# Performance work log

Measured on AMD Instinct MI355X. Metric: run time of the kernel, lower is better.

Reference implementation:

```python
import jax, jax.numpy as jnp
import numpy as np

EPS = 1e-8  # matches torch F.cosine_similarity default eps


def _flatten_spatial(x):
    # [B, C, d, h, w] -> [B, N, C]
    B, C = x.shape[:2]
    return x.reshape(B, C, -1).transpose(0, 2, 1)


def _stage_loss(canon_src, canon_tgt, src_desc, tgt_desc):
    stage_size = src_desc.shape[2:]
    B, C = canon_src.shape[:2]
    # trilinear resize with half-pixel centers == torch align_corners=False
    rs = jax.image.resize(canon_src, (B, C) + stage_size, method='trilinear')
    rt = jax.image.resize(canon_tgt, (B, C) + stage_size, method='trilinear')
    a = _flatten_spatial(rs)  # [B, N, 3]
    b = _flatten_spatial(rt)  # [B, N, 3]
    # squared euclidean distances (argmin is invariant to sqrt)
    a2 = jnp.sum(a * a, axis=-1)  # [B, N]
    b2 = jnp.sum(b * b, axis=-1)  # [B, N]
    ab = jnp.einsum('bnc,bmc->bnm', a, b)  # [B, N, N]
    d2 = a2[:, :, None] + b2[:, None, :] - 2.0 * ab
    nearest = jnp.argmin(d2, axis=-1)  # [B, N] int
    sd = _flatten_spatial(src_desc)  # [B, N, Cd]
    td = _flatten_spatial(tgt_desc)  # [B, N, Cd]
    gathered = jnp.take_along_axis(td, nearest[:, :, None], axis=1)  # [B, N, Cd]
    num = jnp.sum(sd * gathered, axis=-1)
    denom = jnp.maximum(jnp.linalg.norm(sd, axis=-1), EPS) * \
            jnp.maximum(jnp.linalg.norm(gathered, axis=-1), EPS)
    cos = num / denom
    return 1.0 - jnp.mean(cos)


def setup_inputs() -> dict:
    key = jax.random.key(0)
    ks = jax.random.split(key, 6)
    return {
        'canonical_source': jax.random.normal(ks[0], (4, 3, 64, 64, 64), jnp.float32),
        'canonical_target': jax.random.normal(ks[1], (4, 3, 64, 64, 64), jnp.float32),
        'src_desc0': jax.random.normal(ks[2], (4, 32, 16, 16, 16), jnp.float32),
        'tgt_desc0': jax.random.normal(ks[3], (4, 32, 16, 16, 16), jnp.float32),
        'src_desc1': jax.random.normal(ks[4], (4, 32, 8, 8, 8), jnp.float32),
        'tgt_desc1': jax.random.normal(ks[5], (4, 32, 8, 8, 8), jnp.float32),
    }


def reference(canonical_source, canonical_target, src_desc0, tgt_desc0, src_desc1, tgt_desc1):
    l0 = _stage_loss(canonical_source, canonical_target, src_desc0, tgt_desc0)
    l1 = _stage_loss(canonical_source, canonical_target, src_desc1, tgt_desc1)
    return jnp.stack([l0, l1]).mean()
```

## Files before the change

kernel.cpp:

```cpp
#include <hip/hip_runtime.h>
#include <cfloat>

typedef unsigned long long u64;

#define CDESC 32
#define N0 4096
#define N1 512

__device__ __forceinline__ unsigned fbits_mono(float d) {
    unsigned b = __float_as_uint(d);
    return (d >= 0.f) ? (b | 0x80000000u) : ~b;
}

__device__ __forceinline__ void wave_reduce_atomic(float v, float* acc) {
#pragma unroll
    for (int off = 32; off > 0; off >>= 1) v += __shfl_down(v, off, 64);
    if ((threadIdx.x & 63) == 0) atomicAdd(acc, v);
}

__global__ __launch_bounds__(256) void pass1_fused(
        const float* __restrict__ csrc, const float* __restrict__ ctgt,
        const float* __restrict__ sd0, const float* __restrict__ td0,
        const float* __restrict__ sd1, const float* __restrict__ td1,
        float* __restrict__ x16a, float* __restrict__ x16b,
        float* __restrict__ x8a,  float* __restrict__ x8b,
        float* __restrict__ sd0T, float* __restrict__ td0T,
        float* __restrict__ sd1T, float* __restrict__ td1T,
        float* __restrict__ acc) {
    __shared__ __align__(16) float lds[6612];
    float* sRowP = lds;
    float* xf16P = lds + 4672;
    float* xf8P  = lds + 5964;
    const int tid = threadIdx.x;
    const int bx  = blockIdx.x, by = blockIdx.y;
    if (by == 0 && bx == 0 && tid < 4) acc[tid] = 0.f;

    if (bx < 768) {
        int bc = bx >> 6, z = bx & 63;
        const float* in = by ? ctgt : csrc;
        float* o16 = by ? x16b : x16a;
        float* o8  = by ? x8b  : x8a;
        if (tid < 512) {
            int r = tid >> 3, c = tid & 7;
            sRowP[r * 73 + (c < 4 ? c : 64 + c)] = 0.f;
        }
        if (tid < 76) {
            int r = tid / 19, c = tid % 19;
            xf16P[(r < 2 ? r : r + 64) * 19 + c] = 0.f;
        }
        if (tid < 72) {
            int r = tid / 9, c = tid % 9;
            xf8P[(r < 4 ? r : r + 64) * 9 + c] = 0.f;
        }
        const float4* src = (const float4*)(in + (size_t)(bc * 64 + z) * 4096);
#pragma unroll
        for (int k = 0; k < 4; ++k) {
            float4 v = src[tid + k * 256];
            int g = tid + k * 256;
            int y = g >> 4, j = (g & 15) * 4;
            float* p = &sRowP[y * 73 + 4 + j];
            p[0] = v.x; p[1] = v.y; p[2] = v.z; p[3] = v.w;
        }
        __syncthreads();
#pragma unroll
        for (int k = 0; k < 6; ++k) {
            int o = tid + k * 256;
            if (o < 1024) {
                int y = o >> 4, xo = o & 15;
                const float* r = &sRowP[y * 73 + 4 * xo + 2];
                float sum = 0.f;
#pragma unroll
                for (int t = 0; t < 8; ++t) {
                    float w = 1.f - fabsf((float)t - 3.5f) * 0.25f;
                    sum = fmaf(w, r[t], sum);
                }
                float wsum = (xo == 0 || xo == 15) ? 3.5f : 4.0f;
                xf16P[(y + 2) * 19 + xo] = sum / wsum;
            } else {
                int o2 = o - 1024;
                int y = o2 >> 3, xo = o2 & 7;
                const float* r = &sRowP[y * 73 + 8 * xo];
                float sum = 0.f;
#pragma unroll
                for (int t = 0; t < 16; ++t) {
                    float w = 1.f - fabsf((float)t - 7.5f) * 0.125f;
                    sum = fmaf(w, r[t], sum);
                }
                float wsum = (xo == 0 || xo == 7) ? 7.f : 8.f;
                xf8P[(y + 4) * 9 + xo] = sum / wsum;
            }
        }
        __syncthreads();
        {
            int y2 = tid >> 4, x = tid & 15;
            float sum = 0.f;
#pragma unroll
            for (int t = 0; t < 8; ++t) {
                float w = 1.f - fabsf((float)t - 3.5f) * 0.25f;
                sum = fmaf(w, xf16P[(4 * y2 + t) * 19 + x], sum);
            }
            float wsum = (y2 == 0 || y2 == 15) ? 3.5f : 4.0f;
            o16[bc * 16384 + z * 256 + y2 * 16 + x] = sum / wsum;
        }
        if (tid < 64) {
            int y2 = tid >> 3, x = tid & 7;
            float sum = 0.f;
#pragma unroll
            for (int t = 0; t < 16; ++t) {
                float w = 1.f - fabsf((float)t - 7.5f) * 0.125f;
                sum = fmaf(w, xf8P[(8 * y2 + t) * 9 + x], sum);
            }
            float wsum = (y2 == 0 || y2 == 7) ? 7.f : 8.f;
            o8[bc * 4096 + z * 64 + y2 * 8 + x] = sum / wsum;
        }
    } else {
        float* tile = lds;
        int tl = bx - 768;
        const float* din; float* dout; int N, b, n0;
        if (tl < 256) { din = by ? td0 : sd0; dout = by ? td0T : sd0T;
                        N = N0; b = tl >> 6; n0 = (tl & 63) * 64; }
        else { tl -= 256; din = by ? td1 : sd1; dout = by ? td1T : sd1T;
               N = N1; b = tl >> 3; n0 = (tl & 7) * 64; }
#pragma unroll
        for (int i = 0; i < 8; ++i) {
            int idx = tid + i * 256;
            int c = idx >> 6, j = idx & 63;
            tile[j * 33 + c] = din[((size_t)b * CDESC + c) * N + n0 + j];
        }
        __syncthreads();
#pragma unroll
        for (int i = 0; i < 8; ++i) {
            int idx = tid + i * 256;
            int p = idx >> 5, c = idx & 31;
            dout[((size_t)b * N + n0 + p) * CDESC + c] = tile[p * 33 + c];
        }
    }
}

__global__ __launch_bounds__(256) void pass2z(
        const float* __restrict__ x16a, const float* __restrict__ x16b,
        const float* __restrict__ x8a,  const float* __restrict__ x8b,
        float4* __restrict__ ps0, float4* __restrict__ pt0,
        float4* __restrict__ ps1, float4* __restrict__ pt1) {
    int gid = blockIdx.x * 256 + threadIdx.x;
    if (blockIdx.x < 128) {
        int side = gid >> 14, r = gid & 16383;
        int b = r >> 12, n = r & 4095;
        int x = n & 15, y = (n >> 4) & 15, z = n >> 8;
        const float* t = side ? x16b : x16a;
        const float* base = t + (size_t)b * 49152 + y * 16 + x;
        float a0 = 0.f, a1 = 0.f, a2 = 0.f, wzs = 0.f;
#pragma unroll
        for (int tt = 0; tt < 8; ++tt) {
            float w = 1.f - fabsf((float)tt - 3.5f) * 0.25f;
            int jz = 4 * z - 2 + tt;
            if ((unsigned)jz < 64u) {
                const float* p = base + jz * 256;
                a0 = fmaf(w, p[0],     a0);
                a1 = fmaf(w, p[16384], a1);
                a2 = fmaf(w, p[32768], a2);
                wzs += w;
            }
        }
        float inv = 1.f / wzs;
        a0 *= inv; a1 *= inv; a2 *= inv;
        float sq = a0 * a0 + a1 * a1 + a2 * a2;
        if (side) pt0[b * N0 + n] = make_float4(-2.f * a0, -2.f * a1, -2.f * a2, sq);
        else      ps0[b * N0 + n] = make_float4(a0, a1, a2, sq);
    } else {
        int g = gid - 32768;
        int side = g >> 11, r = g & 2047;
        int b = r >> 9, n = r & 511;
        int x = n & 7, y = (n >> 3) & 7, z = n >> 6;
        const float* t = side ? x8b : x8a;
        const float* base = t + (size_t)b * 12288 + y * 8 + x;
        float a0 = 0.f, a1 = 0.f, a2 = 0.f, wzs = 0.f;
#pragma unroll
        for (int tt = 0; tt < 16; ++tt) {
            float w = 1.f - fabsf((float)tt - 7.5f) * 0.125f;
            int jz = 8 * z - 4 + tt;
            if ((unsigned)jz < 64u) {
                const float* p = base + jz * 64;
                a0 = fmaf(w, p[0],    a0);
                a1 = fmaf(w, p[4096], a1);
                a2 = fmaf(w, p[8192], a2);
                wzs += w;
            }
        }
        float inv = 1.f / wzs;
        a0 *= inv; a1 *= inv; a2 *= inv;
        float sq = a0 * a0 + a1 * a1 + a2 * a2;
        if (side) pt1[b * N1 + n] = make_float4(-2.f * a0, -2.f * a1, -2.f * a2, sq);
        else      ps1[b * N1 + n] = make_float4(a0, a1, a2, sq);
    }
}

__device__ __forceinline__ float cos_pm(const float* __restrict__ sT,
                                        const float* __restrict__ tT,
                                        size_t si, size_t ti) {
    const float4* s = (const float4*)(sT + si * CDESC);
    const float4* t = (const float4*)(tT + ti * CDESC);
    float num = 0.f, s2 = 0.f, t2 = 0.f;
#pragma unroll
    for (int c = 0; c < 8; ++c) {
        float4 a = s[c], g = t[c];
        num = fmaf(a.x, g.x, fmaf(a.y, g.y, fmaf(a.z, g.z, fmaf(a.w, g.w, num))));
        s2  = fmaf(a.x, a.x, fmaf(a.y, a.y, fmaf(a.z, a.z, fmaf(a.w, a.w, s2))));
        t2  = fmaf(g.x, g.x, fmaf(g.y, g.y, fmaf(g.z, g.z, fmaf(g.w, g.w, t2))));
    }
    return num / (fmaxf(sqrtf(s2), 1e-8f) * fmaxf(sqrtf(t2), 1e-8f));
}

__device__ __forceinline__ float dist_pm(float4 P, float4 Q) {
    return fmaf(P.x, Q.x, fmaf(P.y, Q.y, fmaf(P.z, Q.z, Q.w)));
}

__global__ __launch_bounds__(256) void nn_cos_all(
        const float4* __restrict__ ps0, const float4* __restrict__ pt0,
        const float* __restrict__ sd0T, const float* __restrict__ td0T,
        const float4* __restrict__ ps1, const float4* __restrict__ pt1,
        const float* __restrict__ sd1T, const float* __restrict__ td1T,
        float* acc, float* __restrict__ out) {
    extern __shared__ __align__(16) char smraw[];
    float4* sm = (float4*)smraw;
    const int tid = threadIdx.x;
    const int bx  = blockIdx.x;

    if (bx < 256) {
        int b = bx >> 6, ptile = bx & 63;
        const float4* tp = pt0 + b * N0;
        for (int i = tid; i < N0; i += 256)
            sm[i] = tp[i];
        __syncthreads();
        int w = tid >> 6, lane = tid & 63;
        int n = ptile * 64 + lane;
        float4 P = ps0[b * N0 + n];
        const int m0 = w * 1024;
        float best = FLT_MAX; int bbase = 0;
        for (int k0 = 0; k0 < 1024; k0 += 16) {
            float d[16];
#pragma unroll
            for (int u = 0; u < 16; ++u)
                d[u] = dist_pm(P, sm[m0 + k0 + u]);
            float e0 = fminf(d[0],  d[1]),  e1 = fminf(d[2],  d[3]);
            float e2 = fminf(d[4],  d[5]),  e3 = fminf(d[6],  d[7]);
            float e4 = fminf(d[8],  d[9]),  e5 = fminf(d[10], d[11]);
            float e6 = fminf(d[12], d[13]), e7 = fminf(d[14], d[15]);
            float f0 = fminf(e0, e1), f1 = fminf(e2, e3);
            float f2 = fminf(e4, e5), f3 = fminf(e6, e7);
            float bm = fminf(fminf(f0, f1), fminf(f2, f3));
            if (bm < best) { best = bm; bbase = k0; }
        }
        int bi = 0;
#pragma unroll
        for (int u = 15; u >= 0; --u) {
            float dv = dist_pm(P, sm[m0 + bbase + u]);
            if (dv == best) bi = u;
        }
        u64 key = ((u64)fbits_mono(best) << 32) | (unsigned)(m0 + bbase + bi);
        __syncthreads();
        u64* keys = (u64*)smraw;
        keys[w * 64 + lane] = key;
        __syncthreads();
        if (tid < 64) {
            u64 k0 = keys[tid],       k1 = keys[tid + 64];
            u64 k2 = keys[tid + 128], k3 = keys[tid + 192];
            u64 ka = k0 < k1 ? k0 : k1;
            u64 kb = k2 < k3 ? k2 : k3;
            u64 kk = ka < kb ? ka : kb;
            int nearest = (int)(unsigned)(kk & 0xFFFFFFFFull);
            int n2 = ptile * 64 + tid;
            float cosv = cos_pm(sd0T, td0T, (size_t)b * N0 + n2,
                                (size_t)b * N0 + nearest);
            wave_reduce_atomic(cosv, acc + 0);
        }
    } else {
        int bb = bx - 256;
        int b = bb >> 1;
        const float4* tp = pt1 + b * N1;
        for (int i = tid; i < N1; i += 256)
            sm[i] = tp[i];
        __syncthreads();
        int n = (bb & 1) * 256 + tid;
        float4 P = ps1[b * N1 + n];
        float best = FLT_MAX; int bbase = 0;
        for (int k0 = 0; k0 < N1; k0 += 16) {
            float d[16];
#pragma unroll
            for (int u = 0; u < 16; ++u)
                d[u] = dist_pm(P, sm[k0 + u]);
            float e0 = fminf(d[0],  d[1]),  e1 = fminf(d[2],  d[3]);
            float e2 = fminf(d[4],  d[5]),  e3 = fminf(d[6],  d[7]);
            float e4 = fminf(d[8],  d[9]),  e5 = fminf(d[10], d[11]);
            float e6 = fminf(d[12], d[13]), e7 = fminf(d[14], d[15]);
            float f0 = fminf(e0, e1), f1 = fminf(e2, e3);
            float f2 = fminf(e4, e5), f3 = fminf(e6, e7);
            float bm = fminf(fminf(f0, f1), fminf(f2, f3));
            if (bm < best) { best = bm; bbase = k0; }
        }
        int bi = 0;
#pragma unroll
        for (int u = 15; u >= 0; --u) {
            float dv = dist_pm(P, sm[bbase + u]);
            if (dv == best) bi = u;
        }
        float cosv = cos_pm(sd1T, td1T, (size_t)b * N1 + n,
                            (size_t)b * N1 + bbase + bi);
        wave_reduce_atomic(cosv, acc + 1);
    }

    __syncthreads();
    if (tid == 0) {
        __threadfence();
        unsigned old = atomicAdd((unsigned*)(acc + 2), 1u);
        if (old == 263u) {
            float a0 = atomicAdd(acc + 0, 0.f);
            float a1 = atomicAdd(acc + 1, 0.f);
            out[0] = 1.f - 0.5f * (a0 * (1.f / 16384.f) + a1 * (1.f / 2048.f));
        }
    }
}

extern "C" void kernel_launch(void* const* d_in, const int* in_sizes, int n_in,
                              void* d_out, int out_size, void* d_ws, size_t ws_size,
                              hipStream_t stream) {
    const float* c_src = (const float*)d_in[0];
    const float* c_tgt = (const float*)d_in[1];
    const float* sd0   = (const float*)d_in[2];
    const float* td0   = (const float*)d_in[3];
    const float* sd1   = (const float*)d_in[4];
    const float* td1   = (const float*)d_in[5];
    float* out = (float*)d_out;

    char* ws = (char*)d_ws;
    float* acc  = (float*)ws;
    float* x16a = (float*)(ws + 256);
    float* x16b = x16a + 196608;
    float* x8a  = x16b + 196608;
    float* x8b  = x8a + 49152;
    float4* ps0 = (float4*)(x8b + 49152);
    float4* pt0 = ps0 + 16384;
    float4* ps1 = pt0 + 16384;
    float4* pt1 = ps1 + 2048;
    float* sd0T = (float*)(pt1 + 2048);
    float* td0T = sd0T + 524288;
    float* sd1T = td0T + 524288;
    float* td1T = sd1T + 65536;

    pass1_fused<<<dim3(1056, 2), 256, 0, stream>>>(c_src, c_tgt, sd0, td0, sd1, td1,
                                                   x16a, x16b, x8a, x8b,
                                                   sd0T, td0T, sd1T, td1T, acc);
    pass2z<<<144, 256, 0, stream>>>(x16a, x16b, x8a, x8b, ps0, pt0, ps1, pt1);
    nn_cos_all<<<264, 256, 65536, stream>>>(ps0, pt0, sd0T, td0T, ps1, pt1,
                                            sd1T, td1T, acc, out);
}
```

Baseline: 114.0 us.

## Split stage-0 NN search across blocks with 4-point register tiling and global atomicMin

Each stage-0 block now loads only a quarter of the target points (1024) into shared memory and has each thread evaluate four source points against one shared Q. This cuts LDS traffic per distance and shrinks dynamic shared memory. Partial argmins are merged through a global 64-bit atomicMin on packed keys, and a per-group ticket counter lets the last arriving block compute the cosine terms. Key and ticket initialization are folded into pass2z. The cost is global atomics and a last-block-done pattern that relies on memory visibility between blocks.

```diff
diff --git a/kernel.cpp b/kernel.cpp
--- a/kernel.cpp
+++ b/kernel.cpp
@@ -141,8 +141,11 @@
         const float* __restrict__ x16a, const float* __restrict__ x16b,
         const float* __restrict__ x8a,  const float* __restrict__ x8b,
         float4* __restrict__ ps0, float4* __restrict__ pt0,
-        float4* __restrict__ ps1, float4* __restrict__ pt1) {
+        float4* __restrict__ ps1, float4* __restrict__ pt1,
+        u64* __restrict__ gkeys, unsigned* __restrict__ gtick) {
     int gid = blockIdx.x * 256 + threadIdx.x;
+    if (gid < 16384) gkeys[gid] = ~0ull;
+    else if (gid < 16448) gtick[gid - 16384] = 0u;
     if (blockIdx.x < 128) {
         int side = gid >> 14, r = gid & 16383;
         int b = r >> 12, n = r & 4095;
@@ -220,56 +223,63 @@
         const float* __restrict__ sd0T, const float* __restrict__ td0T,
         const float4* __restrict__ ps1, const float4* __restrict__ pt1,
         const float* __restrict__ sd1T, const float* __restrict__ td1T,
+        u64* __restrict__ gkeys, unsigned* __restrict__ gtick,
         float* acc, float* __restrict__ out) {
     extern __shared__ __align__(16) char smraw[];
     float4* sm = (float4*)smraw;
+    __shared__ unsigned sflag;
     const int tid = threadIdx.x;
     const int bx  = blockIdx.x;
 
     if (bx < 256) {
-        int b = bx >> 6, ptile = bx & 63;
-        const float4* tp = pt0 + b * N0;
-        for (int i = tid; i < N0; i += 256)
+        int b = bx >> 6, g = (bx >> 2) & 15, q = bx & 3;
+        const float4* tp = pt0 + b * N0 + q * 1024;
+        for (int i = tid; i < 1024; i += 256)
             sm[i] = tp[i];
-        __syncthreads();
-        int w = tid >> 6, lane = tid & 63;
-        int n = ptile * 64 + lane;
-        float4 P = ps0[b * N0 + n];
-        const int m0 = w * 1024;
-        float best = FLT_MAX; int bbase = 0;
-        for (int k0 = 0; k0 < 1024; k0 += 16) {
-            float d[16];
-#pragma unroll
-            for (int u = 0; u < 16; ++u)
-                d[u] = dist_pm(P, sm[m0 + k0 + u]);
-            float e0 = fminf(d[0],  d[1]),  e1 = fminf(d[2],  d[3]);
-            float e2 = fminf(d[4],  d[5]),  e3 = fminf(d[6],  d[7]);
-            float e4 = fminf(d[8],  d[9]),  e5 = fminf(d[10], d[11]);
-            float e6 = fminf(d[12], d[13]), e7 = fminf(d[14], d[15]);
-            float f0 = fminf(e0, e1), f1 = fminf(e2, e3);
-            float f2 = fminf(e4, e5), f3 = fminf(e6, e7);
-            float bm = fminf(fminf(f0, f1), fminf(f2, f3));
-            if (bm < best) { best = bm; bbase = k0; }
-        }
-        int bi = 0;
-#pragma unroll
-        for (int u = 15; u >= 0; --u) {
-            float dv = dist_pm(P, sm[m0 + bbase + u]);
-            if (dv == best) bi = u;
-        }
-        u64 key = ((u64)fbits_mono(best) << 32) | (unsigned)(m0 + bbase + bi);
-        __syncthreads();
-        u64* keys = (u64*)smraw;
-        keys[w * 64 + lane] = key;
-        __syncthreads();
-        if (tid < 64) {
-            u64 k0 = keys[tid],       k1 = keys[tid + 64];
-            u64 k2 = keys[tid + 128], k3 = keys[tid + 192];
+        int lane = tid & 63, w = tid >> 6;
+        int pbase = b * N0 + g * 256 + lane;
+        float4 P0 = ps0[pbase];
+        float4 P1 = ps0[pbase + 64];
+        float4 P2 = ps0[pbase + 128];
+        float4 P3 = ps0[pbase + 192];
+        __syncthreads();
+        const int m0 = w * 256;
+        float b0 = FLT_MAX, b1 = FLT_MAX, b2 = FLT_MAX, b3 = FLT_MAX;
+        int i0 = 0, i1 = 0, i2 = 0, i3 = 0;
+#pragma unroll 8
+        for (int k = 0; k < 256; ++k) {
+            float4 Q = sm[m0 + k];
+            float d0 = dist_pm(P0, Q);
+            float d1 = dist_pm(P1, Q);
+            float d2 = dist_pm(P2, Q);
+            float d3 = dist_pm(P3, Q);
+            if (d0 < b0) { b0 = d0; i0 = k; }
+            if (d1 < b1) { b1 = d1; i1 = k; }
+            if (d2 < b2) { b2 = d2; i2 = k; }
+            if (d3 < b3) { b3 = d3; i3 = k; }
+        }
+        int mb = q * 1024 + m0;
+        u64* keys = (u64*)(smraw + 16384);
+        keys[w * 256 + lane      ] = ((u64)fbits_mono(b0) << 32) | (unsigned)(mb + i0);
+        keys[w * 256 + lane + 64 ] = ((u64)fbits_mono(b1) << 32) | (unsigned)(mb + i1);
+        keys[w * 256 + lane + 128] = ((u64)fbits_mono(b2) << 32) | (unsigned)(mb + i2);
+        keys[w * 256 + lane + 192] = ((u64)fbits_mono(b3) << 32) | (unsigned)(mb + i3);
+        __syncthreads();
+        {
+            u64 k0 = keys[tid],       k1 = keys[256 + tid];
+            u64 k2 = keys[512 + tid], k3 = keys[768 + tid];
             u64 ka = k0 < k1 ? k0 : k1;
             u64 kb = k2 < k3 ? k2 : k3;
             u64 kk = ka < kb ? ka : kb;
+            atomicMin(&gkeys[(size_t)b * N0 + g * 256 + tid], kk);
+        }
+        __syncthreads();
+        if (tid == 0) sflag = atomicAdd(&gtick[b * 16 + g], 1u);
+        __syncthreads();
+        if (sflag == 3u) {
+            u64 kk = atomicAdd(&gkeys[(size_t)b * N0 + g * 256 + tid], 0ull);
             int nearest = (int)(unsigned)(kk & 0xFFFFFFFFull);
-            int n2 = ptile * 64 + tid;
+            int n2 = g * 256 + tid;
             float cosv = cos_pm(sd0T, td0T, (size_t)b * N0 + n2,
                                 (size_t)b * N0 + nearest);
             wave_reduce_atomic(cosv, acc + 0);
@@ -346,11 +356,14 @@
     float* td0T = sd0T + 524288;
     float* sd1T = td0T + 524288;
     float* td1T = sd1T + 65536;
+    u64* gkeys  = (u64*)(td1T + 65536);
+    unsigned* gtick = (unsigned*)(gkeys + 16384);
 
     pass1_fused<<<dim3(1056, 2), 256, 0, stream>>>(c_src, c_tgt, sd0, td0, sd1, td1,
                                                    x16a, x16b, x8a, x8b,
                                                    sd0T, td0T, sd1T, td1T, acc);
-    pass2z<<<144, 256, 0, stream>>>(x16a, x16b, x8a, x8b, ps0, pt0, ps1, pt1);
-    nn_cos_all<<<264, 256, 65536, stream>>>(ps0, pt0, sd0T, td0T, ps1, pt1,
-                                            sd1T, td1T, acc, out);
-}
+    pass2z<<<144, 256, 0, stream>>>(x16a, x16b, x8a, x8b, ps0, pt0, ps1, pt1,
+                                    gkeys, gtick);
+    nn_cos_all<<<264, 256, 24576, stream>>>(ps0, pt0, sd0T, td0T, ps1, pt1,
+                                            sd1T, td1T, gkeys, gtick, acc, out);
+}
```

After: 111.7 us. 2.0% less time.
